# Optimization experiments

Measured on AMD Instinct MI355X. Metric: run time of the kernel, lower is better.

## Reference

```python
import jax, jax.numpy as jnp
import numpy as np

BN_EPS = 1e-5


def ball_query(pos, radius, k):
    """PointNet++-style ball query: for each point, the first k point indices
    (in index order) whose distance < radius; shorter lists are padded with the
    first valid index (self is always valid since dist=0). pos: (b,n,3).
    Returns idx: (b,n,k) int32."""
    b, n, _ = pos.shape
    sq = jnp.sum(pos * pos, axis=-1)                       # (b,n)
    d2 = sq[:, :, None] + sq[:, None, :] - 2.0 * jnp.einsum('bnc,bmc->bnm', pos, pos)
    mask = d2 < radius * radius                            # (b,n,n)
    cand = jnp.where(mask, jnp.arange(n, dtype=jnp.int32)[None, None, :], jnp.int32(n))
    # smallest-k indices in ascending order == first-k valid in index order
    neg_top, _ = jax.lax.top_k(-cand, k)                   # (b,n,k)
    idx = -neg_top
    first = idx[..., :1]
    idx = jnp.where(idx == n, first, idx)                  # pad with first neighbor
    return idx


def reference(pos, x, w1, gamma, beta, w2, b2, radius, k):
    pos = jax.lax.stop_gradient(pos)
    idx = ball_query(pos, radius, k)                       # (b,n,k)
    grouped = jax.vmap(lambda p, i: p[i])(pos, idx)        # (b,n,k,3)
    rel = grouped - pos[:, :, None, :]                     # center-subtract
    # 1x1 conv (3->3, no bias)
    h = jnp.einsum('bnkc,dc->bnkd', rel, w1)
    # BatchNorm2d (training-mode batch stats over b,k,n per channel)
    mean = jnp.mean(h, axis=(0, 1, 2))
    var = jnp.mean((h - mean) ** 2, axis=(0, 1, 2))
    h = (h - mean) * jax.lax.rsqrt(var + BN_EPS) * gamma + beta
    h = jax.nn.relu(h)
    # 1x1 conv (3->out_channel) + bias
    pe = jnp.einsum('bnkd,ed->bnke', h, w2) + b2           # (b,n,k,C)
    pe = jnp.max(pe, axis=2)                               # max over k neighbors
    return x + pe


def setup_inputs() -> dict:
    key = jax.random.key(0)
    ks = jax.random.split(key, 5)
    b, n, c, kk = 2, 8192, 64, 32
    pos = jax.random.uniform(ks[0], (b, n, 3), dtype=jnp.float32)
    x = jax.random.normal(ks[1], (b, n, c), dtype=jnp.float32)
    w1 = jax.random.normal(ks[2], (3, 3), dtype=jnp.float32) * 0.5
    gamma = jnp.ones((3,), dtype=jnp.float32)
    beta = jnp.zeros((3,), dtype=jnp.float32)
    w2 = jax.random.normal(ks[3], (c, 3), dtype=jnp.float32) * 0.5
    b2 = jnp.zeros((c,), dtype=jnp.float32)
    radius = jnp.float32(0.1)
    return {"pos": pos, "x": x, "w1": w1, "gamma": gamma, "beta": beta,
            "w2": w2, "b2": b2, "radius": radius, "k": kk}
```

## Files before the change

kernel.cpp:

```cpp
#include <hip/hip_runtime.h>
#include <math.h>

#define NPTS   8192
#define NBATCH 2
#define NQ     (NPTS * NBATCH)
#define KNB    32
#define CFEAT  64
#define BN_EPS 1e-5f

#define MAXC     1000
#define CSTR     1024
#define CAP_HIT  128
#define ACC_SCALE 16777216.0

#define QBK2  16
#define NBLK2 (NQ / QBK2)

#define QBK3  16
#define NBLK3 (NQ / QBK3)

#define WS_H     0
#define WS_ACC   (WS_H + NQ * 3 * KNB)
#define WS_CS    (WS_ACC + 12)
#define WS_BIN   (WS_CS + 2 * CSTR)

__device__ __forceinline__ int grid_from_r(double rd) {
    int G = (int)(1.0 / rd);
    if (G < 1) G = 1;
    while (G > 1 && 1.0 / (double)G < rd) --G;
    if (G > 10) G = 10;
    return G;
}

__device__ __forceinline__ int mbcnt64(unsigned long long m) {
    return (int)__builtin_amdgcn_mbcnt_hi((unsigned)(m >> 32),
             __builtin_amdgcn_mbcnt_lo((unsigned)m, 0u));
}

__device__ __forceinline__ int cell_of(float v, float Gf, int G) {
    int c = (int)(v * Gf);
    return c > G - 1 ? G - 1 : c;
}

__global__ __launch_bounds__(1024) void kBin(
    const float* __restrict__ pos, const float* __restrict__ radius,
    float* __restrict__ ws)
{
    __shared__ int hist[MAXC];
    __shared__ int cur[MAXC];
    __shared__ int wtot[16];

    const int tid = threadIdx.x, lane = tid & 63, wave = tid >> 6;
    const int batch = blockIdx.x;
    if (batch == 0 && tid < 6)
        ((long long*)(ws + WS_ACC))[tid] = 0LL;

    const float* bpos = pos + (size_t)batch * NPTS * 3;
    const double rd = (double)radius[0];
    const int G = grid_from_r(rd);
    const float Gf = (float)G;
    const int NC = G * G * G;

    for (int c = tid; c < NC; c += 1024) hist[c] = 0;
    __syncthreads();

    for (int p = tid; p < NPTS; p += 1024) {
        const float* pp = bpos + (size_t)p * 3;
        int c = (cell_of(pp[2], Gf, G) * G + cell_of(pp[1], Gf, G)) * G
                + cell_of(pp[0], Gf, G);
        atomicAdd(&hist[c], 1);
    }
    __syncthreads();

    int v = (tid < NC) ? hist[tid] : 0;
    int incl = v;
#pragma unroll
    for (int off = 1; off < 64; off <<= 1) {
        int t = __shfl_up(incl, off);
        if (lane >= off) incl += t;
    }
    if (lane == 63) wtot[wave] = incl;
    __syncthreads();
    int base = 0;
#pragma unroll
    for (int w = 0; w < 16; ++w) base += (w < wave) ? wtot[w] : 0;
    const int excl = base + incl - v;
    int* cs = (int*)ws + WS_CS + batch * CSTR;
    if (tid < NC) { cs[tid] = excl; cur[tid] = excl; }
    if (tid == 0) cs[NC] = NPTS;
    __syncthreads();

    float4* bin = (float4*)(ws + WS_BIN) + (size_t)batch * NPTS;
    for (int p = tid; p < NPTS; p += 1024) {
        const float* pp = bpos + (size_t)p * 3;
        float x = pp[0], y = pp[1], z = pp[2];
        int c = (cell_of(z, Gf, G) * G + cell_of(y, Gf, G)) * G
                + cell_of(x, Gf, G);
        int slot = atomicAdd(&cur[c], 1);
        bin[slot] = make_float4(x, y, z, __int_as_float(p));
    }
}

__global__ __launch_bounds__(1024) void k2_query(
    const float* __restrict__ pos, const float* __restrict__ w1,
    const float* __restrict__ radius, float* __restrict__ ws)
{
    __shared__ int   hitl[QBK2][CAP_HIT];
    __shared__ int   seli[QBK2][KNB];
    __shared__ float sred[QBK2][6];

    const int tid = threadIdx.x, lane = tid & 63, wave = tid >> 6;
    const int qbase = blockIdx.x * QBK2;
    const int batch = qbase / NPTS;
    const float* bpos = pos + (size_t)batch * NPTS * 3;
    const double rd  = (double)radius[0];
    const double r2d = rd * rd;
    const int G = grid_from_r(rd);
    const float Gf = (float)G;
    const int* cs = (const int*)ws + WS_CS + batch * CSTR;
    const float4* bin = (const float4*)(ws + WS_BIN) + (size_t)batch * NPTS;

    const int qg = qbase + wave;
    const int ql = qg - batch * NPTS;
    const float qx = bpos[ql * 3], qy = bpos[ql * 3 + 1], qz = bpos[ql * 3 + 2];
    const double qxd = (double)qx, qyd = (double)qy, qzd = (double)qz;
    const double qsd = fma(qzd, qzd, fma(qyd, qyd, qxd * qxd));
    const int cx = cell_of(qx, Gf, G);
    const int cy = cell_of(qy, Gf, G);
    const int cz = cell_of(qz, Gf, G);
    const int cx0 = max(cx - 1, 0), cx1 = min(cx + 1, G - 1);

    int rs0[9], rpref[10];
    int tot = 0;
#pragma unroll
    for (int r = 0; r < 9; ++r) {
        const int ny = cy + (r % 3) - 1;
        const int nz = cz + (r / 3) - 1;
        int s0 = 0, len = 0;
        if (ny >= 0 && ny < G && nz >= 0 && nz < G) {
            const int cb = (nz * G + ny) * G;
            s0  = cs[cb + cx0];
            len = cs[cb + cx1 + 1] - s0;
        }
        rs0[r] = s0; rpref[r] = tot; tot += len;
    }
    rpref[9] = tot;
    int del[9];
#pragma unroll
    for (int i = 0; i < 9; ++i) del[i] = rs0[i] - rpref[i];

    const int nw = (tot + 63) >> 6;
    int hc = 0;
    float4 P;
    {
        const int flat = lane;
        int ss = flat + del[0];
#pragma unroll
        for (int i = 1; i < 9; ++i)
            ss += (flat >= rpref[i]) ? (del[i] - del[i - 1]) : 0;
        P = bin[(flat < tot) ? ss : 0];
    }
    for (int w = 0; w < nw; ++w) {
        const float4 Pc = P;
        const int flat = (w << 6) + lane;
        if (w + 1 < nw) {
            const int fn = ((w + 1) << 6) + lane;
            int ssn = fn + del[0];
#pragma unroll
            for (int i = 1; i < 9; ++i)
                ssn += (fn >= rpref[i]) ? (del[i] - del[i - 1]) : 0;
            P = bin[(fn < tot) ? ssn : 0];
        }
        const bool act = flat < tot;
        double xj = (double)Pc.x, yj = (double)Pc.y, zj = (double)Pc.z;
        double sqj = fma(zj, zj, fma(yj, yj, xj * xj));
        double dot = fma(zj, qzd, fma(yj, qyd, xj * qxd));
        double dd  = (qsd + sqj) - 2.0 * dot;
        bool in = act && (dd < r2d);
        unsigned long long bal = __ballot(in);
        if (in) {
            int p2 = hc + mbcnt64(bal);
            if (p2 < CAP_HIT) hitl[wave][p2] = __float_as_int(Pc.w);
        }
        hc += (int)__popcll(bal);
    }
    if (hc > CAP_HIT) hc = CAP_HIT;

    if (hc <= KNB) {
        int v = (lane < hc) ? hitl[wave][lane] : 0x7FFFFFFF;
        int mn = v;
#pragma unroll
        for (int off = 32; off; off >>= 1) mn = min(mn, __shfl_xor(mn, off));
        if (lane < KNB) seli[wave][lane] = (lane < hc) ? v : mn;
    } else {
        int a = (lane < hc) ? hitl[wave][lane] : 0x7FFFFFFF;
        int b = (64 + lane < hc) ? hitl[wave][64 + lane] : 0x7FFFFFFF;
        int lo = 0, hi = NPTS - 1;
        while (lo < hi) {
            int mid = (lo + hi) >> 1;
            int c1 = (int)__popcll(__ballot(a <= mid)) +
                     (int)__popcll(__ballot(b <= mid));
            if (c1 >= KNB) hi = mid; else lo = mid + 1;
        }
        const int t = lo;
        unsigned long long ba = __ballot(a <= t);
        unsigned long long bb = __ballot(b <= t);
        int na = (int)__popcll(ba);
        if (a <= t) seli[wave][mbcnt64(ba)] = a;
        if (b <= t) seli[wave][na + mbcnt64(bb)] = b;
    }

    float w1r[9];
#pragma unroll
    for (int i = 0; i < 9; ++i) w1r[i] = w1[i];

    float ls0 = 0.f, ls1 = 0.f, ls2 = 0.f;
    float lq0 = 0.f, lq1 = 0.f, lq2 = 0.f;
    if (lane < KNB) {
        int j = seli[wave][lane];
        const float* pj = bpos + (size_t)j * 3;
        float rx = __fsub_rn(pj[0], qx);
        float ry = __fsub_rn(pj[1], qy);
        float rz = __fsub_rn(pj[2], qz);
        float h0 = fmaf(rz, w1r[2], fmaf(ry, w1r[1], __fmul_rn(rx, w1r[0])));
        float h1 = fmaf(rz, w1r[5], fmaf(ry, w1r[4], __fmul_rn(rx, w1r[3])));
        float h2 = fmaf(rz, w1r[8], fmaf(ry, w1r[7], __fmul_rn(rx, w1r[6])));
        float* hout = ws + WS_H + (size_t)qg * 3 * KNB;
        hout[0 * KNB + lane] = h0;
        hout[1 * KNB + lane] = h1;
        hout[2 * KNB + lane] = h2;
        ls0 = h0; ls1 = h1; ls2 = h2;
        lq0 = h0 * h0; lq1 = h1 * h1; lq2 = h2 * h2;
    }

#pragma unroll
    for (int m = 1; m < 64; m <<= 1) {
        ls0 += __shfl_xor(ls0, m); ls1 += __shfl_xor(ls1, m); ls2 += __shfl_xor(ls2, m);
        lq0 += __shfl_xor(lq0, m); lq1 += __shfl_xor(lq1, m); lq2 += __shfl_xor(lq2, m);
    }
    if (lane == 0) {
        sred[wave][0] = ls0; sred[wave][1] = ls1; sred[wave][2] = ls2;
        sred[wave][3] = lq0; sred[wave][4] = lq1; sred[wave][5] = lq2;
    }
    __syncthreads();
    if (tid < 6) {
        float s = 0.f;
#pragma unroll
        for (int w = 0; w < QBK2; ++w) s += sred[w][tid];
        long long q = (long long)llrint((double)s * ACC_SCALE);
        atomicAdd((unsigned long long*)(ws + WS_ACC) + tid,
                  (unsigned long long)q);
    }
}

__global__ __launch_bounds__(256) void k3_mlp(
    const float* __restrict__ ws, const float* __restrict__ gamma,
    const float* __restrict__ beta, const float* __restrict__ w2,
    const float* __restrict__ b2, const float* __restrict__ x,
    float* __restrict__ out)
{
    __shared__ float gl[QBK3 * 96];

    const int tid = threadIdx.x;
    const long long* acc = (const long long*)(ws + WS_ACC);
    const double N = (double)((long long)NQ * KNB);
    float ms[3], is[3];
#pragma unroll
    for (int d = 0; d < 3; ++d) {
        double s  = (double)acc[d]     / ACC_SCALE;
        double sq = (double)acc[3 + d] / ACC_SCALE;
        double mean = s / N;
        double var  = sq / N - mean * mean;
        ms[d] = (float)mean;
        is[d] = (float)(1.0 / sqrt(var + (double)BN_EPS));
    }
    const float m0 = ms[0], m1 = ms[1], m2 = ms[2];
    const float i0 = is[0], i1 = is[1], i2 = is[2];
    const float g0 = gamma[0], g1 = gamma[1], g2 = gamma[2];
    const float b0 = beta[0],  b1 = beta[1],  b2c = beta[2];

    const int qbase = blockIdx.x * QBK3;
    const float* hin = ws + WS_H + (size_t)qbase * 96;

#pragma unroll
    for (int r = 0; r < 6; ++r) {
        const int idx = r * 256 + tid;
        const int c = (idx % 96) >> 5;
        float h = hin[idx];
        float mm = c == 0 ? m0 : (c == 1 ? m1 : m2);
        float ii = c == 0 ? i0 : (c == 1 ? i1 : i2);
        float gg = c == 0 ? g0 : (c == 1 ? g1 : g2);
        float bb = c == 0 ? b0 : (c == 1 ? b1 : b2c);
        float n = __fadd_rn(__fmul_rn(__fmul_rn(__fsub_rn(h, mm), ii), gg), bb);
        gl[idx] = fmaxf(n, 0.0f);
    }
    __syncthreads();

    const int ch = tid & 63;
    const int qh = tid >> 6;
    const float w20 = w2[ch * 3 + 0];
    const float w21 = w2[ch * 3 + 1];
    const float w22 = w2[ch * 3 + 2];
    const float bias = b2[ch];

#pragma unroll
    for (int r = 0; r < 4; ++r) {
        const int q = r * 4 + qh;
        const float* gq = &gl[q * 96];
        float m = -INFINITY;
#pragma unroll 4
        for (int kk = 0; kk < KNB; ++kk) {
            float ga = gq[kk], gb = gq[32 + kk], gc = gq[64 + kk];
            float pe = __fadd_rn(fmaf(gc, w22, fmaf(gb, w21, __fmul_rn(ga, w20))), bias);
            m = fmaxf(m, pe);
        }
        const size_t o = (size_t)(qbase + q) * CFEAT + ch;
        out[o] = __fadd_rn(x[o], m);
    }
}

extern "C" void kernel_launch(void* const* d_in, const int* in_sizes, int n_in,
                              void* d_out, int out_size, void* d_ws, size_t ws_size,
                              hipStream_t stream) {
    (void)in_sizes; (void)n_in; (void)out_size; (void)ws_size;
    const float* pos    = (const float*)d_in[0];
    const float* x      = (const float*)d_in[1];
    const float* w1     = (const float*)d_in[2];
    const float* gamma  = (const float*)d_in[3];
    const float* beta   = (const float*)d_in[4];
    const float* w2     = (const float*)d_in[5];
    const float* b2     = (const float*)d_in[6];
    const float* radius = (const float*)d_in[7];
    float* out = (float*)d_out;
    float* ws  = (float*)d_ws;

    hipLaunchKernelGGL(kBin,     dim3(NBATCH), dim3(1024), 0, stream, pos, radius, ws);
    hipLaunchKernelGGL(k2_query, dim3(NBLK2),  dim3(1024), 0, stream, pos, w1, radius, ws);
    hipLaunchKernelGGL(k3_mlp,   dim3(NBLK3),  dim3(256),  0, stream,
                       ws, gamma, beta, w2, b2, x, out);
}
```

Baseline: 56.13 us.

## Use fp32 distance test with fp64 fallback near radius boundary in ball query

```diff
diff --git a/kernel.cpp b/kernel.cpp
--- a/kernel.cpp
+++ b/kernel.cpp
@@ -13,7 +13,7 @@
 #define CAP_HIT  128
 #define ACC_SCALE 16777216.0
 
-#define QBK2  16
+#define QBK2  8
 #define NBLK2 (NQ / QBK2)
 
 #define QBK3  16
@@ -97,11 +97,14 @@
         int c = (cell_of(z, Gf, G) * G + cell_of(y, Gf, G)) * G
                 + cell_of(x, Gf, G);
         int slot = atomicAdd(&cur[c], 1);
-        bin[slot] = make_float4(x, y, z, __int_as_float(p));
-    }
-}
-
-__global__ __launch_bounds__(1024) void k2_query(
+        float sq = fmaf(z, z, fmaf(y, y, x * x));
+        float4 e = make_float4(-2.0f * x, -2.0f * y, -2.0f * z, sq);
+        bin[slot] = e;
+        ((int*)(ws + WS_BIN) + 2 * NPTS * 4)[batch * NPTS + slot] = p;
+    }
+}
+
+__global__ __launch_bounds__(512) void k2_query(
     const float* __restrict__ pos, const float* __restrict__ w1,
     const float* __restrict__ radius, float* __restrict__ ws)
 {
@@ -115,16 +118,18 @@
     const float* bpos = pos + (size_t)batch * NPTS * 3;
     const double rd  = (double)radius[0];
     const double r2d = rd * rd;
+    const float  r2lo = (float)(r2d - 1e-5);
+    const float  r2hi = (float)(r2d + 1e-5);
     const int G = grid_from_r(rd);
     const float Gf = (float)G;
     const int* cs = (const int*)ws + WS_CS + batch * CSTR;
     const float4* bin = (const float4*)(ws + WS_BIN) + (size_t)batch * NPTS;
+    const int* bidx = (int*)(ws + WS_BIN) + 2 * NPTS * 4 + batch * NPTS;
 
     const int qg = qbase + wave;
     const int ql = qg - batch * NPTS;
     const float qx = bpos[ql * 3], qy = bpos[ql * 3 + 1], qz = bpos[ql * 3 + 2];
-    const double qxd = (double)qx, qyd = (double)qy, qzd = (double)qz;
-    const double qsd = fma(qzd, qzd, fma(qyd, qyd, qxd * qxd));
+    const float qsq = fmaf(qz, qz, fmaf(qy, qy, qx * qx));
     const int cx = cell_of(qx, Gf, G);
     const int cy = cell_of(qy, Gf, G);
     const int cz = cell_of(qz, Gf, G);
@@ -151,17 +156,17 @@
 
     const int nw = (tot + 63) >> 6;
     int hc = 0;
-    float4 P;
+    float4 P; int S;
     {
-        const int flat = lane;
-        int ss = flat + del[0];
+        int ss = lane + del[0];
 #pragma unroll
         for (int i = 1; i < 9; ++i)
-            ss += (flat >= rpref[i]) ? (del[i] - del[i - 1]) : 0;
-        P = bin[(flat < tot) ? ss : 0];
+            ss += (lane >= rpref[i]) ? (del[i] - del[i - 1]) : 0;
+        S = (lane < tot) ? ss : 0;
+        P = bin[S];
     }
     for (int w = 0; w < nw; ++w) {
-        const float4 Pc = P;
+        const float4 Pc = P; const int Sc = S;
         const int flat = (w << 6) + lane;
         if (w + 1 < nw) {
             const int fn = ((w + 1) << 6) + lane;
@@ -169,18 +174,31 @@
 #pragma unroll
             for (int i = 1; i < 9; ++i)
                 ssn += (fn >= rpref[i]) ? (del[i] - del[i - 1]) : 0;
-            P = bin[(fn < tot) ? ssn : 0];
+            S = (fn < tot) ? ssn : 0;
+            P = bin[S];
         }
         const bool act = flat < tot;
-        double xj = (double)Pc.x, yj = (double)Pc.y, zj = (double)Pc.z;
-        double sqj = fma(zj, zj, fma(yj, yj, xj * xj));
-        double dot = fma(zj, qzd, fma(yj, qyd, xj * qxd));
-        double dd  = (qsd + sqj) - 2.0 * dot;
-        bool in = act && (dd < r2d);
-        unsigned long long bal = __ballot(in);
+        float d2 = qsq + fmaf(Pc.x, qx, fmaf(Pc.y, qy, fmaf(Pc.z, qz, Pc.w)));
+        bool hi = act && (d2 < r2hi);
+        bool lo = act && (d2 < r2lo);
+        unsigned long long bhi = __ballot(hi);
+        unsigned long long blo = __ballot(lo);
+        unsigned long long bal; bool in;
+        if (bhi != blo) {
+            double xj = (double)Pc.x * -0.5;
+            double yj = (double)Pc.y * -0.5;
+            double zj = (double)Pc.z * -0.5;
+            double sqj = fma(zj, zj, fma(yj, yj, xj * xj));
+            double qxd = (double)qx, qyd = (double)qy, qzd = (double)qz;
+            double qsd = fma(qzd, qzd, fma(qyd, qyd, qxd * qxd));
+            double dot = fma(zj, qzd, fma(yj, qyd, xj * qxd));
+            double dd  = (qsd + sqj) - 2.0 * dot;
+            in  = act && (dd < r2d);
+            bal = __ballot(in);
+        } else { in = lo; bal = blo; }
         if (in) {
             int p2 = hc + mbcnt64(bal);
-            if (p2 < CAP_HIT) hitl[wave][p2] = __float_as_int(Pc.w);
+            if (p2 < CAP_HIT) hitl[wave][p2] = bidx[Sc];
         }
         hc += (int)__popcll(bal);
     }
@@ -195,14 +213,14 @@
     } else {
         int a = (lane < hc) ? hitl[wave][lane] : 0x7FFFFFFF;
         int b = (64 + lane < hc) ? hitl[wave][64 + lane] : 0x7FFFFFFF;
-        int lo = 0, hi = NPTS - 1;
-        while (lo < hi) {
-            int mid = (lo + hi) >> 1;
+        int lo2 = 0, hi2 = NPTS - 1;
+        while (lo2 < hi2) {
+            int mid = (lo2 + hi2) >> 1;
             int c1 = (int)__popcll(__ballot(a <= mid)) +
                      (int)__popcll(__ballot(b <= mid));
-            if (c1 >= KNB) hi = mid; else lo = mid + 1;
-        }
-        const int t = lo;
+            if (c1 >= KNB) hi2 = mid; else lo2 = mid + 1;
+        }
+        const int t = lo2;
         unsigned long long ba = __ballot(a <= t);
         unsigned long long bb = __ballot(b <= t);
         int na = (int)__popcll(ba);
@@ -335,7 +353,7 @@
     float* ws  = (float*)d_ws;
 
     hipLaunchKernelGGL(kBin,     dim3(NBATCH), dim3(1024), 0, stream, pos, radius, ws);
-    hipLaunchKernelGGL(k2_query, dim3(NBLK2),  dim3(1024), 0, stream, pos, w1, radius, ws);
+    hipLaunchKernelGGL(k2_query, dim3(NBLK2),  dim3(512),  0, stream, pos, w1, radius, ws);
     hipLaunchKernelGGL(k3_mlp,   dim3(NBLK3),  dim3(256),  0, stream,
                        ws, gamma, beta, w2, b2, x, out);
 }
```

Measured after the change: 76.97 us. 37.1% more time.
